# Kernel tuning notes

Hardware: AMD Instinct MI355X
Metric: run time of the kernel (lower is better)

Reference implementation:

```python
import jax, jax.numpy as jnp
import numpy as np

N = 40000          # nodes
E = 640000         # edges (avg degree 16)
IN_F = 128
OUT_F = 128
DIST_DIM = 32
N_BOUND = 32       # embedding table has N_BOUND+1 rows


def _xavier(key, shape):
    fan_in, fan_out = shape
    std = (2.0 / (fan_in + fan_out)) ** 0.5
    return jax.random.normal(key, shape, jnp.float32) * std


def setup_inputs() -> dict:
    key = jax.random.key(0)
    ks = jax.random.split(key, 12)
    feat = jax.random.normal(ks[0], (N, IN_F), jnp.float32)
    loc = jax.random.uniform(ks[1], (N, 2), jnp.float32) * 10.0
    src = jax.random.randint(ks[2], (E,), 0, N)
    dst = jax.random.randint(ks[3], (E,), 0, N)
    inter_ids = jax.random.randint(ks[4], (E,), 0, N)
    # weights stored [in, out] (torch Linear weight transposed)
    W_fc = _xavier(ks[5], (IN_F, OUT_F))
    Wq = _xavier(ks[6], (OUT_F, OUT_F))
    Wk = _xavier(ks[7], (OUT_F, OUT_F))
    Wq2 = _xavier(ks[8], (2 * OUT_F, OUT_F))
    Wk2 = _xavier(ks[9], (2 * OUT_F, OUT_F))
    G_w = _xavier(ks[10], (DIST_DIM, OUT_F))
    embed = jax.random.normal(ks[11], (N_BOUND + 1, DIST_DIM), jnp.float32)
    boundaries = jnp.linspace(0.45, 14.4, N_BOUND).astype(jnp.float32)
    return dict(feat=feat, loc=loc, W_fc=W_fc, Wq=Wq, Wk=Wk, Wq2=Wq2,
                Wk2=Wk2, G_w=G_w, embed=embed, boundaries=boundaries,
                src=src, dst=dst, inter_ids=inter_ids)


def reference(feat, loc, W_fc, Wq, Wk, Wq2, Wk2, G_w, embed, boundaries,
              src, dst, inter_ids):
    scale = jnp.sqrt(jnp.float32(OUT_F))
    h = feat @ W_fc                               # [N, OUT_F]  (feat_h)

    f_src = feat[src]                             # [E, IN_F]
    f_dst = feat[dst]                             # [E, IN_F]

    # attention score e1 (the only score the source module actually uses)
    q = f_dst @ Wq                                # [E, OUT_F]
    k = f_src @ Wk                                # [E, OUT_F]
    e = jnp.sum(q * k, axis=1) / scale            # [E]

    # --- e2 branch: computed by the source but discarded (returns only 'e': e1).
    # Reproduced for fidelity; XLA dead-code-eliminates it.
    inter_pos = loc[inter_ids]
    dist1 = jnp.linalg.norm(loc[dst] - loc[src], axis=1)
    dist_ = jnp.linalg.norm(loc[src] - inter_pos, axis=1)
    de1 = embed[jnp.searchsorted(boundaries, dist1, side='left')] @ G_w
    de_ = embed[jnp.searchsorted(boundaries, dist_, side='left')] @ G_w
    q2 = jnp.concatenate([f_src, de1], axis=1) @ Wq2
    k2 = jnp.concatenate([feat[inter_ids], de_], axis=1) @ Wk2
    _e2 = jnp.sum(q2 * k2, axis=1) / scale        # unused, as in source
    # ---

    # edge_softmax: segmented softmax over incoming edges of each dst node
    e_max = jax.ops.segment_max(e, dst, num_segments=N)      # [N]
    ex = jnp.exp(e - e_max[dst])                              # [E]
    denom = jax.ops.segment_sum(ex, dst, num_segments=N)     # [N]
    a = ex / denom[dst]                                       # [E]

    # u_mul_e + sum: out[v] = sum_{(u->v)} h[u] * a_uv
    msgs = h[src] * a[:, None]                                # [E, OUT_F]
    rst = jax.ops.segment_sum(msgs, dst, num_segments=N)     # [N, OUT_F]
    return rst
```

## Files before the change

### kernel.cpp

```cpp
#include <hip/hip_runtime.h>
#include <hip/hip_bf16.h>

#define NN 40000
#define NE 640000
#define FDIM 128

typedef __attribute__((ext_vector_type(4))) float f32x4;
typedef __attribute__((ext_vector_type(8))) short bf16x8;

__device__ inline float bflo(unsigned int w) { return __uint_as_float(w << 16); }
__device__ inline float bfhi(unsigned int w) { return __uint_as_float(w & 0xffff0000u); }
__device__ inline unsigned short f2bf(float x) {
  __hip_bfloat16 b = __float2bfloat16(x);
  return *(unsigned short*)&b;
}

__global__ __launch_bounds__(256) void prep_k(const float* __restrict__ feat,
                                              const float* __restrict__ w0,
                                              const float* __restrict__ w1,
                                              const float* __restrict__ w2,
                                              unsigned short* __restrict__ feat_bf,
                                              unsigned short* __restrict__ Wt,
                                              const int* __restrict__ src,
                                              const int* __restrict__ dst,
                                              int* __restrict__ pos,
                                              int* __restrict__ csr) {
  const int b = blockIdx.x, t = threadIdx.x;
  if (b < 5000) {
    int i = b * 256 + t;
    float4 v = ((const float4*)feat)[i];
    ushort4 r;
    r.x = f2bf(v.x); r.y = f2bf(v.y); r.z = f2bf(v.z); r.w = f2bf(v.w);
    ((ushort4*)feat_bf)[i] = r;
  } else if (b < 5003) {
    const int m = b - 5000;
    const float* w = (m == 0) ? w0 : (m == 1) ? w1 : w2;
    unsigned short* o = Wt + m * 16384;
    for (int idx = t; idx < 16384; idx += 256) {
      int k = idx >> 7, c = idx & 127;
      o[c * 128 + k] = f2bf(w[idx]);
    }
  } else {
    int e = (b - 5003) * 256 + t;
    if (e < NE) {
      int v = dst[e];
      int slot = atomicAdd(&pos[v], 1);
      if (slot < 64) csr[v * 64 + slot] = src[e];
    }
  }
}

__global__ __launch_bounds__(256) void gemm3_k(const unsigned short* __restrict__ feat,
                                               const unsigned short* __restrict__ wt_all,
                                               unsigned short* __restrict__ Qb,
                                               unsigned short* __restrict__ KH) {
  __shared__ unsigned short sA[64][136];
  __shared__ unsigned short sB[128][136];
  const int bx = blockIdx.x, by = blockIdx.y;
  const unsigned short* wt = wt_all + by * 16384;
  const int t = threadIdx.x;
  const int rbase = bx * 64;

  const uint4* fa = (const uint4*)(feat + (size_t)rbase * FDIM);
  #pragma unroll
  for (int i = 0; i < 4; ++i) {
    int idx = t + i * 256;
    uint4 v = fa[idx];
    *(uint4*)&sA[idx >> 4][(idx & 15) << 3] = v;
  }
  const uint4* wb = (const uint4*)wt;
  #pragma unroll
  for (int i = 0; i < 8; ++i) {
    int idx = t + i * 256;
    uint4 v = wb[idx];
    *(uint4*)&sB[idx >> 4][(idx & 15) << 3] = v;
  }
  __syncthreads();

  const int l = t & 63;
  const int w = t >> 6;
  const int r16 = l & 15;
  const int kb = (l >> 4) << 3;
  f32x4 acc[8];
  #pragma unroll
  for (int ch = 0; ch < 8; ++ch) acc[ch] = (f32x4){0.f, 0.f, 0.f, 0.f};

  #pragma unroll
  for (int ks = 0; ks < 4; ++ks) {
    const int k0 = ks * 32 + kb;
    bf16x8 a = *(const bf16x8*)&sA[w * 16 + r16][k0];
    #pragma unroll
    for (int ch = 0; ch < 8; ++ch) {
      bf16x8 b = *(const bf16x8*)&sB[ch * 16 + r16][k0];
      acc[ch] = __builtin_amdgcn_mfma_f32_16x16x32_bf16(a, b, acc[ch], 0, 0, 0);
    }
  }
  const int orow = rbase + w * 16 + ((l >> 4) << 2);
  const int ocol = l & 15;
  const float scl = (by == 1) ? 0.08838834764831845f : 1.0f;
  unsigned short* ob;
  int stride, off;
  if (by == 1) { ob = Qb; stride = 128; off = 0; }
  else         { ob = KH; stride = 256; off = (by == 0) ? 128 : 0; }
  #pragma unroll
  for (int ch = 0; ch < 8; ++ch) {
    #pragma unroll
    for (int r = 0; r < 4; ++r) {
      ob[(size_t)(orow + r) * stride + off + ch * 16 + ocol] = f2bf(acc[ch][r] * scl);
    }
  }
}

__global__ __launch_bounds__(256) void node_k(const unsigned int* __restrict__ Qb,
                                              const char* __restrict__ KH,
                                              const int* __restrict__ deg,
                                              const int* __restrict__ csr,
                                              float* __restrict__ out) {
  const int v = blockIdx.x * 4 + (threadIdx.x >> 6);
  const int l = threadIdx.x & 63;
  const int g = l >> 4;
  const int i = l & 15;

  const uint4 qw = *(const uint4*)((const char*)Qb + (size_t)v * 256 + i * 16);
  float qf[8];
  qf[0] = bflo(qw.x); qf[1] = bfhi(qw.x); qf[2] = bflo(qw.y); qf[3] = bfhi(qw.y);
  qf[4] = bflo(qw.z); qf[5] = bfhi(qw.z); qf[6] = bflo(qw.w); qf[7] = bfhi(qw.w);

  int d_ = deg[v];
  d_ = (d_ > 64) ? 64 : d_;
  float m = -3.0e38f, den = 0.f;
  float acc[8];
  #pragma unroll
  for (int j = 0; j < 8; ++j) acc[j] = 0.f;

  const int T = (d_ + 3) >> 2;
  const int* cbase = csr + v * 64;
  for (int t = 0; t < T; ++t) {
    const int eidx = 4 * t + g;
    const bool act = eidx < d_;
    const int u = act ? cbase[eidx] : 0;
    const char* row = KH + (size_t)u * 512;
    const uint4 kw = *(const uint4*)(row + i * 16);
    const uint4 hw = *(const uint4*)(row + 256 + i * 16);
    float s = qf[0] * bflo(kw.x) + qf[1] * bfhi(kw.x)
            + qf[2] * bflo(kw.y) + qf[3] * bfhi(kw.y)
            + qf[4] * bflo(kw.z) + qf[5] * bfhi(kw.z)
            + qf[6] * bflo(kw.w) + qf[7] * bfhi(kw.w);
    s += __shfl_xor(s, 1); s += __shfl_xor(s, 2);
    s += __shfl_xor(s, 4); s += __shfl_xor(s, 8);
    const float mn = act ? fmaxf(m, s) : m;
    const float f = __expf(m - mn);
    const float p = act ? __expf(s - mn) : 0.f;
    den = den * f + p;
    acc[0] = acc[0] * f + p * bflo(hw.x); acc[1] = acc[1] * f + p * bfhi(hw.x);
    acc[2] = acc[2] * f + p * bflo(hw.y); acc[3] = acc[3] * f + p * bfhi(hw.y);
    acc[4] = acc[4] * f + p * bflo(hw.z); acc[5] = acc[5] * f + p * bfhi(hw.z);
    acc[6] = acc[6] * f + p * bflo(hw.w); acc[7] = acc[7] * f + p * bfhi(hw.w);
    m = mn;
  }

  #pragma unroll
  for (int off = 16; off < 64; off <<= 1) {
    const float m2 = __shfl_xor(m, off);
    const float den2 = __shfl_xor(den, off);
    const float mn = fmaxf(m, m2);
    const float f1 = __expf(m - mn);
    const float f2 = __expf(m2 - mn);
    den = den * f1 + den2 * f2;
    #pragma unroll
    for (int j = 0; j < 8; ++j) {
      const float a2 = __shfl_xor(acc[j], off);
      acc[j] = acc[j] * f1 + a2 * f2;
    }
    m = mn;
  }

  if (g == 0) {
    const float inv = (d_ > 0) ? 1.0f / den : 0.f;
    float4 r0, r1;
    r0.x = acc[0] * inv; r0.y = acc[1] * inv; r0.z = acc[2] * inv; r0.w = acc[3] * inv;
    r1.x = acc[4] * inv; r1.y = acc[5] * inv; r1.z = acc[6] * inv; r1.w = acc[7] * inv;
    float* ob = out + (size_t)v * 128 + i * 8;
    *(float4*)ob = r0;
    *(float4*)(ob + 4) = r1;
  }
}

extern "C" void kernel_launch(void* const* d_in, const int* in_sizes, int n_in,
                              void* d_out, int out_size, void* d_ws, size_t ws_size,
                              hipStream_t stream) {
  const float* feat = (const float*)d_in[0];
  const float* W_fc = (const float*)d_in[2];
  const float* Wq   = (const float*)d_in[3];
  const float* Wk   = (const float*)d_in[4];
  const int* src = (const int*)d_in[10];
  const int* dst = (const int*)d_in[11];

  char* ws = (char*)d_ws;
  unsigned short* feat_bf = (unsigned short*)(ws);
  unsigned short* Wt      = (unsigned short*)(ws + 10240000);
  unsigned short* Qb      = (unsigned short*)(ws + 10338304);
  unsigned short* KH      = (unsigned short*)(ws + 20578304);
  int* pos = (int*)(ws + 41058304);
  int* csr = (int*)(ws + 41222144);

  hipMemsetAsync(pos, 0, NN * sizeof(int), stream);
  prep_k<<<7503, 256, 0, stream>>>(feat, W_fc, Wq, Wk, feat_bf, Wt, src, dst, pos, csr);
  dim3 g(625, 3);
  gemm3_k<<<g, 256, 0, stream>>>(feat_bf, Wt, Qb, KH);
  node_k<<<10000, 256, 0, stream>>>((const unsigned int*)Qb, (const char*)KH,
                                    pos, csr, (float*)d_out);
}
```

Measured before the change: 205.0 us.

## Fuse feat conversion into GEMM, interleave CSR fill, two-pass softmax in node kernel

The separate feat-to-bf16 pass is removed: the GEMM blocks now load fp32 feat and convert it while staging into shared memory. The CSR-building atomics are interleaved into the same launch as the GEMM blocks, and the memset is replaced by zeroing inside the weight-prep kernel. The node kernel now computes all scores first, takes the max, then accumulates without online rescaling. This also drops the rescaling during the cross-group combine. Together these cut a launch, a full intermediate round trip and the exp work per edge, at the cost of more registers for the unrolled 16-slot arrays and three redundant fp32 feat reads across the GEMM blocks.

New measurement: 200.4 us. 2.3% less time.

```diff
diff --git a/kernel.cpp b/kernel.cpp
--- a/kernel.cpp
+++ b/kernel.cpp
@@ -3,7 +3,6 @@
 
 #define NN 40000
 #define NE 640000
-#define FDIM 128
 
 typedef __attribute__((ext_vector_type(4))) float f32x4;
 typedef __attribute__((ext_vector_type(8))) short bf16x8;
@@ -15,63 +14,63 @@
   return *(unsigned short*)&b;
 }
 
-__global__ __launch_bounds__(256) void prep_k(const float* __restrict__ feat,
-                                              const float* __restrict__ w0,
-                                              const float* __restrict__ w1,
-                                              const float* __restrict__ w2,
-                                              unsigned short* __restrict__ feat_bf,
-                                              unsigned short* __restrict__ Wt,
-                                              const int* __restrict__ src,
-                                              const int* __restrict__ dst,
-                                              int* __restrict__ pos,
-                                              int* __restrict__ csr) {
+__global__ __launch_bounds__(256) void k0_prep(const float* __restrict__ w0,
+                                               const float* __restrict__ w1,
+                                               const float* __restrict__ w2,
+                                               unsigned short* __restrict__ Wt,
+                                               int* __restrict__ pos) {
   const int b = blockIdx.x, t = threadIdx.x;
-  if (b < 5000) {
-    int i = b * 256 + t;
-    float4 v = ((const float4*)feat)[i];
-    ushort4 r;
-    r.x = f2bf(v.x); r.y = f2bf(v.y); r.z = f2bf(v.z); r.w = f2bf(v.w);
-    ((ushort4*)feat_bf)[i] = r;
-  } else if (b < 5003) {
-    const int m = b - 5000;
-    const float* w = (m == 0) ? w0 : (m == 1) ? w1 : w2;
-    unsigned short* o = Wt + m * 16384;
+  if (b < 3) {
+    const float* w = (b == 0) ? w0 : (b == 1) ? w1 : w2;
+    unsigned short* o = Wt + b * 16384;
     for (int idx = t; idx < 16384; idx += 256) {
       int k = idx >> 7, c = idx & 127;
       o[c * 128 + k] = f2bf(w[idx]);
     }
   } else {
-    int e = (b - 5003) * 256 + t;
-    if (e < NE) {
-      int v = dst[e];
-      int slot = atomicAdd(&pos[v], 1);
-      if (slot < 64) csr[v * 64 + slot] = src[e];
-    }
-  }
-}
-
-__global__ __launch_bounds__(256) void gemm3_k(const unsigned short* __restrict__ feat,
-                                               const unsigned short* __restrict__ wt_all,
-                                               unsigned short* __restrict__ Qb,
-                                               unsigned short* __restrict__ KH) {
+    ((int4*)pos)[(b - 3) * 256 + t] = (int4){0, 0, 0, 0};
+  }
+}
+
+__global__ __launch_bounds__(256) void k1_gemm_fill(const float* __restrict__ feat,
+                                                    const unsigned short* __restrict__ wt_all,
+                                                    unsigned short* __restrict__ Qb,
+                                                    unsigned short* __restrict__ KH,
+                                                    const int* __restrict__ src,
+                                                    const int* __restrict__ dst,
+                                                    int* __restrict__ pos,
+                                                    int* __restrict__ csr) {
   __shared__ unsigned short sA[64][136];
   __shared__ unsigned short sB[128][136];
-  const int bx = blockIdx.x, by = blockIdx.y;
+  const int bid = blockIdx.x, t = threadIdx.x;
+  const int r7 = bid % 7, k7 = bid / 7;
+
+  if (r7 >= 3) {
+    const int e = (k7 * 4 + (r7 - 3)) * 256 + t;
+    const int v = dst[e];
+    const int slot = atomicAdd(&pos[v], 1);
+    if (slot < 64) csr[v * 64 + slot] = src[e];
+    return;
+  }
+
+  const int gi = k7 * 3 + r7;
+  const int by = gi / 625, bx = gi % 625;
   const unsigned short* wt = wt_all + by * 16384;
-  const int t = threadIdx.x;
   const int rbase = bx * 64;
 
-  const uint4* fa = (const uint4*)(feat + (size_t)rbase * FDIM);
-  #pragma unroll
-  for (int i = 0; i < 4; ++i) {
-    int idx = t + i * 256;
-    uint4 v = fa[idx];
-    *(uint4*)&sA[idx >> 4][(idx & 15) << 3] = v;
+  const float4* fa = (const float4*)(feat + (size_t)rbase * 128);
+  #pragma unroll
+  for (int j = 0; j < 8; ++j) {
+    int idx = t + j * 256;
+    float4 v = fa[idx];
+    ushort4 r;
+    r.x = f2bf(v.x); r.y = f2bf(v.y); r.z = f2bf(v.z); r.w = f2bf(v.w);
+    *(ushort4*)&sA[idx >> 5][(idx & 31) << 2] = r;
   }
   const uint4* wb = (const uint4*)wt;
   #pragma unroll
-  for (int i = 0; i < 8; ++i) {
-    int idx = t + i * 256;
+  for (int j = 0; j < 8; ++j) {
+    int idx = t + j * 256;
     uint4 v = wb[idx];
     *(uint4*)&sB[idx >> 4][(idx & 15) << 3] = v;
   }
@@ -111,7 +110,7 @@
   }
 }
 
-__global__ __launch_bounds__(256) void node_k(const unsigned int* __restrict__ Qb,
+__global__ __launch_bounds__(256) void node_k(const char* __restrict__ Qb,
                                               const char* __restrict__ KH,
                                               const int* __restrict__ deg,
                                               const int* __restrict__ csr,
@@ -121,58 +120,65 @@
   const int g = l >> 4;
   const int i = l & 15;
 
-  const uint4 qw = *(const uint4*)((const char*)Qb + (size_t)v * 256 + i * 16);
+  const uint4 qw = *(const uint4*)(Qb + (size_t)v * 256 + i * 16);
   float qf[8];
   qf[0] = bflo(qw.x); qf[1] = bfhi(qw.x); qf[2] = bflo(qw.y); qf[3] = bfhi(qw.y);
   qf[4] = bflo(qw.z); qf[5] = bfhi(qw.z); qf[6] = bflo(qw.w); qf[7] = bfhi(qw.w);
 
   int d_ = deg[v];
   d_ = (d_ > 64) ? 64 : d_;
-  float m = -3.0e38f, den = 0.f;
+  const int* cbase = csr + v * 64;
+
+  float s[16];
+  int us[16];
+  #pragma unroll
+  for (int t = 0; t < 16; ++t) {
+    const int eidx = 4 * t + g;
+    float sv = -3.0e38f;
+    int u = 0;
+    if (eidx < d_) {
+      u = cbase[eidx];
+      const uint4 kw = *(const uint4*)(KH + (size_t)u * 512 + i * 16);
+      float sd = qf[0] * bflo(kw.x) + qf[1] * bfhi(kw.x)
+               + qf[2] * bflo(kw.y) + qf[3] * bfhi(kw.y)
+               + qf[4] * bflo(kw.z) + qf[5] * bfhi(kw.z)
+               + qf[6] * bflo(kw.w) + qf[7] * bfhi(kw.w);
+      sd += __shfl_xor(sd, 1); sd += __shfl_xor(sd, 2);
+      sd += __shfl_xor(sd, 4); sd += __shfl_xor(sd, 8);
+      sv = sd;
+    }
+    s[t] = sv;
+    us[t] = u;
+  }
+
+  float m = s[0];
+  #pragma unroll
+  for (int t = 1; t < 16; ++t) m = fmaxf(m, s[t]);
+  m = fmaxf(m, __shfl_xor(m, 16));
+  m = fmaxf(m, __shfl_xor(m, 32));
+
+  float den = 0.f;
   float acc[8];
   #pragma unroll
   for (int j = 0; j < 8; ++j) acc[j] = 0.f;
-
-  const int T = (d_ + 3) >> 2;
-  const int* cbase = csr + v * 64;
-  for (int t = 0; t < T; ++t) {
-    const int eidx = 4 * t + g;
-    const bool act = eidx < d_;
-    const int u = act ? cbase[eidx] : 0;
-    const char* row = KH + (size_t)u * 512;
-    const uint4 kw = *(const uint4*)(row + i * 16);
-    const uint4 hw = *(const uint4*)(row + 256 + i * 16);
-    float s = qf[0] * bflo(kw.x) + qf[1] * bfhi(kw.x)
-            + qf[2] * bflo(kw.y) + qf[3] * bfhi(kw.y)
-            + qf[4] * bflo(kw.z) + qf[5] * bfhi(kw.z)
-            + qf[6] * bflo(kw.w) + qf[7] * bfhi(kw.w);
-    s += __shfl_xor(s, 1); s += __shfl_xor(s, 2);
-    s += __shfl_xor(s, 4); s += __shfl_xor(s, 8);
-    const float mn = act ? fmaxf(m, s) : m;
-    const float f = __expf(m - mn);
-    const float p = act ? __expf(s - mn) : 0.f;
-    den = den * f + p;
-    acc[0] = acc[0] * f + p * bflo(hw.x); acc[1] = acc[1] * f + p * bfhi(hw.x);
-    acc[2] = acc[2] * f + p * bflo(hw.y); acc[3] = acc[3] * f + p * bfhi(hw.y);
-    acc[4] = acc[4] * f + p * bflo(hw.z); acc[5] = acc[5] * f + p * bfhi(hw.z);
-    acc[6] = acc[6] * f + p * bflo(hw.w); acc[7] = acc[7] * f + p * bfhi(hw.w);
-    m = mn;
+  #pragma unroll
+  for (int t = 0; t < 16; ++t) {
+    if (4 * t + g < d_) {
+      const uint4 hw = *(const uint4*)(KH + (size_t)us[t] * 512 + 256 + i * 16);
+      const float p = __expf(s[t] - m);
+      den += p;
+      acc[0] += p * bflo(hw.x); acc[1] += p * bfhi(hw.x);
+      acc[2] += p * bflo(hw.y); acc[3] += p * bfhi(hw.y);
+      acc[4] += p * bflo(hw.z); acc[5] += p * bfhi(hw.z);
+      acc[6] += p * bflo(hw.w); acc[7] += p * bfhi(hw.w);
+    }
   }
 
   #pragma unroll
   for (int off = 16; off < 64; off <<= 1) {
-    const float m2 = __shfl_xor(m, off);
-    const float den2 = __shfl_xor(den, off);
-    const float mn = fmaxf(m, m2);
-    const float f1 = __expf(m - mn);
-    const float f2 = __expf(m2 - mn);
-    den = den * f1 + den2 * f2;
+    den += __shfl_xor(den, off);
     #pragma unroll
-    for (int j = 0; j < 8; ++j) {
-      const float a2 = __shfl_xor(acc[j], off);
-      acc[j] = acc[j] * f1 + a2 * f2;
-    }
-    m = mn;
+    for (int j = 0; j < 8; ++j) acc[j] += __shfl_xor(acc[j], off);
   }
 
   if (g == 0) {
@@ -197,17 +203,14 @@
   const int* dst = (const int*)d_in[11];
 
   char* ws = (char*)d_ws;
-  unsigned short* feat_bf = (unsigned short*)(ws);
-  unsigned short* Wt      = (unsigned short*)(ws + 10240000);
-  unsigned short* Qb      = (unsigned short*)(ws + 10338304);
-  unsigned short* KH      = (unsigned short*)(ws + 20578304);
-  int* pos = (int*)(ws + 41058304);
-  int* csr = (int*)(ws + 41222144);
-
-  hipMemsetAsync(pos, 0, NN * sizeof(int), stream);
-  prep_k<<<7503, 256, 0, stream>>>(feat, W_fc, Wq, Wk, feat_bf, Wt, src, dst, pos, csr);
-  dim3 g(625, 3);
-  gemm3_k<<<g, 256, 0, stream>>>(feat_bf, Wt, Qb, KH);
-  node_k<<<10000, 256, 0, stream>>>((const unsigned int*)Qb, (const char*)KH,
+  unsigned short* Wt = (unsigned short*)(ws);
+  unsigned short* Qb = (unsigned short*)(ws + 98304);
+  unsigned short* KH = (unsigned short*)(ws + 10338304);
+  int* pos = (int*)(ws + 30818304);
+  int* csr = (int*)(ws + 30982144);
+
+  k0_prep<<<43, 256, 0, stream>>>(W_fc, Wq, Wk, Wt, pos);
+  k1_gemm_fill<<<4375, 256, 0, stream>>>(feat, Wt, Qb, KH, src, dst, pos, csr);
+  node_k<<<10000, 256, 0, stream>>>((const char*)Qb, (const char*)KH,
                                     pos, csr, (float*)d_out);
 }
```
